# Performance work log

Hardware: AMD Instinct MI355X
Metric: run time of the kernel (lower is better)

Reference implementation:

```python
import jax, jax.numpy as jnp
import numpy as np

HID = 768          # args.hidden_size
LSTM2 = 768        # args.lstm_dim * 2
SCALE = HID ** -0.5


def _cross_attn(q_in, kv_in, Wq, bq, Wk, bk, Wv, bv):
    # Linear projections (weights stored as [in, out])
    Q = q_in @ Wq + bq            # [B, Sq, H]
    K = kv_in @ Wk + bk           # [B, Sk, H]
    V = kv_in @ Wv + bv           # [B, Sk, H]
    attn = jnp.einsum('bqh,bkh->bqk', Q, K) * SCALE
    attn = jax.nn.softmax(attn, axis=-1)
    return jnp.einsum('bqk,bkh->bqh', attn, V)


def setup_inputs() -> dict:
    key = jax.random.key(0)
    ks = jax.random.split(key, 14)
    B, Ssyn, Ssem = 4, 4096, 2048
    syntactic_feat = jax.random.normal(ks[0], (B, Ssyn, LSTM2), jnp.float32)
    semantic_feat = jax.random.normal(ks[1], (B, Ssem, HID), jnp.float32)

    def lin(k, fan_in, fan_out):
        kw, kb = jax.random.split(k)
        bound = 1.0 / np.sqrt(fan_in)
        W = jax.random.uniform(kw, (fan_in, fan_out), jnp.float32, -bound, bound)
        b = jax.random.uniform(kb, (fan_out,), jnp.float32, -bound, bound)
        return W, b

    # syntax_to_semantic: query_dim=HID, key_dim=LSTM2
    Wq1, bq1 = lin(ks[2], HID, HID)
    Wk1, bk1 = lin(ks[3], LSTM2, HID)
    Wv1, bv1 = lin(ks[4], LSTM2, HID)
    # semantic_to_syntax: query_dim=LSTM2, key_dim=HID
    Wq2, bq2 = lin(ks[5], LSTM2, HID)
    Wk2, bk2 = lin(ks[6], HID, HID)
    Wv2, bv2 = lin(ks[7], HID, HID)
    return dict(syntactic_feat=syntactic_feat, semantic_feat=semantic_feat,
                Wq1=Wq1, bq1=bq1, Wk1=Wk1, bk1=bk1, Wv1=Wv1, bv1=bv1,
                Wq2=Wq2, bq2=bq2, Wk2=Wk2, bk2=bk2, Wv2=Wv2, bv2=bv2)


def reference(syntactic_feat, semantic_feat,
              Wq1, bq1, Wk1, bk1, Wv1, bv1,
              Wq2, bq2, Wk2, bk2, Wv2, bv2):
    # enhanced_semantic: queries from semantic, keys/values from syntactic
    enhanced_semantic = _cross_attn(semantic_feat, syntactic_feat,
                                    Wq1, bq1, Wk1, bk1, Wv1, bv1)
    # enhanced_syntax: queries from syntactic, keys/values from semantic
    enhanced_syntax = _cross_attn(syntactic_feat, semantic_feat,
                                  Wq2, bq2, Wk2, bk2, Wv2, bv2)
    return enhanced_semantic, enhanced_syntax
```

## Files before the change

### kernel.cpp

```cpp
#include <hip/hip_runtime.h>
#include <stdint.h>


typedef unsigned short u16;
typedef __attribute__((ext_vector_type(8))) __bf16 bf16x8;
typedef __attribute__((ext_vector_type(4))) float f32x4;

__device__ __forceinline__ float bf2f(u16 u) {
  union { unsigned int i; float f; } x; x.i = ((unsigned int)u) << 16; return x.f;
}
__device__ __forceinline__ u16 f2bf(float f) {
  union { float f; unsigned int i; } x; x.f = f;
  unsigned int i = x.i;
  i += 0x7fffu + ((i >> 16) & 1u);
  return (u16)(i >> 16);
}

__device__ __forceinline__ void cp16(void* lds, const void* g) {
  __builtin_amdgcn_global_load_lds((__attribute__((address_space(1))) void*)g,
                                   (__attribute__((address_space(3))) void*)lds,
                                   16, 0, 0);
}

struct GemmDesc {
  const u16* A; const u16* Bt; const float* bias; void* C;
  long sA, sB, sC;
  int K, lda, ldb, ldc;
  int gx, gy;
  int start;
  int mode, outf;
  float scale;
};
struct GemmPack { GemmDesc d[6]; int nd; };

__global__ __launch_bounds__(256)
void gemm_multi_kernel(GemmPack p)
{
  __shared__ __align__(16) u16 Asl[128 * 64];
  __shared__ __align__(16) u16 Bsl[128 * 64];

  int seg = 0;
#pragma unroll
  for (int t = 1; t < 6; ++t)
    if (t < p.nd && (int)blockIdx.x >= p.d[t].start) seg = t;
  const GemmDesc& g = p.d[seg];
  const int local = (int)blockIdx.x - g.start;
  const int pxy = g.gx * g.gy;
  const int bz = local / pxy;
  const int rem = local - bz * pxy;
  const int by = rem / g.gx;
  const int bx = rem - by * g.gx;

  const int tid  = threadIdx.x;
  const int lane = tid & 63;
  const int wave = tid >> 6;
  const int l15  = lane & 15;
  const int quad = lane >> 4;
  const int mw   = (wave >> 1) * 64;
  const int nw   = (wave & 1) * 64;

  const char* Ab = (const char*)(g.A + (long)bz * g.sA + (long)bx * 128 * g.lda);
  const char* Bb = (const char*)(g.Bt + (long)bz * g.sB + (long)by * 128 * g.ldb);

  const int srow  = wave * 8 + (lane >> 3);
  const int gchk  = (lane & 7) ^ (lane >> 3);
  const long ldaB = (long)g.lda * 2;
  const long ldbB = (long)g.ldb * 2;
  const char* pa00 = Ab + (long)srow * ldaB + (gchk << 4);
  const char* pb00 = Bb + (long)srow * ldbB + (gchk << 4);
  char* ldsA = (char*)Asl + wave * 1024;
  char* ldsB = (char*)Bsl + wave * 1024;

  int ia[2][4], ib[2][4];
#pragma unroll
  for (int s = 0; s < 2; ++s)
#pragma unroll
    for (int i = 0; i < 4; ++i) {
      const int m = mw + i * 16 + l15;
      ia[s][i] = m * 8 + ((s * 4 + quad) ^ (l15 & 7));
      const int n = nw + i * 16 + l15;
      ib[s][i] = n * 8 + ((s * 4 + quad) ^ (l15 & 7));
    }

  f32x4 acc[4][4];
  {
    f32x4 zz = {0.f, 0.f, 0.f, 0.f};
#pragma unroll
    for (int i = 0; i < 4; ++i)
#pragma unroll
      for (int j = 0; j < 4; ++j) acc[i][j] = zz;
  }

  const int nk = g.K >> 6;
  for (int kk = 0; kk < nk; ++kk) {
    const long kb = (long)kk << 7;
#pragma unroll
    for (int r = 0; r < 4; ++r) {
      cp16(ldsA + r * 4096, pa00 + kb + (long)r * 32 * ldaB);
      cp16(ldsB + r * 4096, pb00 + kb + (long)r * 32 * ldbB);
    }
    __syncthreads();

    const bf16x8* As8 = (const bf16x8*)Asl;
    const bf16x8* Bs8 = (const bf16x8*)Bsl;
#pragma unroll
    for (int s = 0; s < 2; ++s) {
      bf16x8 a[4], b[4];
#pragma unroll
      for (int i = 0; i < 4; ++i) a[i] = As8[ia[s][i]];
#pragma unroll
      for (int j = 0; j < 4; ++j) b[j] = Bs8[ib[s][j]];
#pragma unroll
      for (int i = 0; i < 4; ++i)
#pragma unroll
        for (int j = 0; j < 4; ++j)
          acc[i][j] = __builtin_amdgcn_mfma_f32_16x16x32_bf16(b[j], a[i], acc[i][j], 0, 0, 0);
    }
    __syncthreads();
  }

  const long cbase = (long)bz * g.sC;
#pragma unroll
  for (int i = 0; i < 4; ++i) {
    const int row = bx * 128 + mw + i * 16 + l15;
    const float rbias = (g.mode == 2) ? g.bias[row] : 0.f;
#pragma unroll
    for (int j = 0; j < 4; ++j) {
      const int colbase = by * 128 + nw + j * 16 + quad * 4;
      float v[4];
#pragma unroll
      for (int r = 0; r < 4; ++r) v[r] = acc[i][j][r] * g.scale;
      if (g.mode == 1) {
        const float4 cb = *(const float4*)(g.bias + colbase);
        v[0] += cb.x; v[1] += cb.y; v[2] += cb.z; v[3] += cb.w;
      } else if (g.mode == 2) {
#pragma unroll
        for (int r = 0; r < 4; ++r) v[r] += rbias;
      }
      const long idx = cbase + (long)row * g.ldc + colbase;
      if (g.outf) {
        float4 st; st.x = v[0]; st.y = v[1]; st.z = v[2]; st.w = v[3];
        *(float4*)((float*)g.C + idx) = st;
      } else {
        uint2 st;
        st.x = (unsigned int)f2bf(v[0]) | ((unsigned int)f2bf(v[1]) << 16);
        st.y = (unsigned int)f2bf(v[2]) | ((unsigned int)f2bf(v[3]) << 16);
        *(uint2*)((u16*)g.C + idx) = st;
      }
    }
  }
}

__global__ __launch_bounds__(256)
void cvt2_bf16_kernel(const float* __restrict__ sa, u16* __restrict__ da, int n8a,
                      const float* __restrict__ sb, u16* __restrict__ db, int n8b)
{
  int idx = blockIdx.x * 256 + threadIdx.x;
  const float* src; u16* dst; int i;
  if (idx < n8a) { src = sa; dst = da; i = idx; }
  else           { src = sb; dst = db; i = idx - n8a; if (i >= n8b) return; }
  const float4* s4 = (const float4*)src;
  float4 a = s4[i * 2], b = s4[i * 2 + 1];
  uint4 o;
  o.x = (unsigned int)f2bf(a.x) | ((unsigned int)f2bf(a.y) << 16);
  o.y = (unsigned int)f2bf(a.z) | ((unsigned int)f2bf(a.w) << 16);
  o.z = (unsigned int)f2bf(b.x) | ((unsigned int)f2bf(b.y) << 16);
  o.w = (unsigned int)f2bf(b.z) | ((unsigned int)f2bf(b.w) << 16);
  ((uint4*)dst)[i] = o;
}

__global__ void transpose6_kernel(const float* s0, const float* s1, const float* s2,
                                  const float* s3, const float* s4, const float* s5,
                                  u16* d0, u16* d1, u16* d2,
                                  u16* d3, u16* d4, u16* d5)
{
  __shared__ float t[32][33];
  const float* src; u16* dst;
  switch (blockIdx.z) {
    case 0: src = s0; dst = d0; break;
    case 1: src = s1; dst = d1; break;
    case 2: src = s2; dst = d2; break;
    case 3: src = s3; dst = d3; break;
    case 4: src = s4; dst = d4; break;
    default: src = s5; dst = d5; break;
  }
  const int tx = threadIdx.x, ty = threadIdx.y;
  const int x = blockIdx.x * 32 + tx;
  const int y0 = blockIdx.y * 32;
#pragma unroll
  for (int j = 0; j < 32; j += 8) t[ty + j][tx] = src[(long)(y0 + ty + j) * 768 + x];
  __syncthreads();
  const int x2 = y0 + tx;
#pragma unroll
  for (int j = 0; j < 32; j += 8)
    dst[(long)(blockIdx.x * 32 + ty + j) * 768 + x2] = f2bf(t[tx][ty + j]);
}

template <int NV>
__device__ __forceinline__ void softmax_row(u16* row)
{
  __shared__ float red[8];
  const int tid  = threadIdx.x;
  const int lane = tid & 63;
  const int wave = tid >> 6;
  uint4* p4 = (uint4*)row;

  uint4 ld[NV / 8];
#pragma unroll
  for (int c = 0; c < NV / 8; ++c) ld[c] = p4[tid + c * 256];
  float v[NV];
#pragma unroll
  for (int c = 0; c < NV / 8; ++c) {
    unsigned int w[4] = {ld[c].x, ld[c].y, ld[c].z, ld[c].w};
#pragma unroll
    for (int q = 0; q < 4; ++q) {
      v[c * 8 + q * 2]     = bf2f((u16)(w[q] & 0xffffu));
      v[c * 8 + q * 2 + 1] = bf2f((u16)(w[q] >> 16));
    }
  }

  float m = -1e30f;
#pragma unroll
  for (int i = 0; i < NV; ++i) m = fmaxf(m, v[i]);
#pragma unroll
  for (int off = 32; off > 0; off >>= 1) m = fmaxf(m, __shfl_xor(m, off, 64));
  if (lane == 0) red[wave] = m;
  __syncthreads();
  m = fmaxf(fmaxf(red[0], red[1]), fmaxf(red[2], red[3]));

  float s = 0.f;
#pragma unroll
  for (int i = 0; i < NV; ++i) { v[i] = __expf(v[i] - m); s += v[i]; }
#pragma unroll
  for (int off = 32; off > 0; off >>= 1) s += __shfl_xor(s, off, 64);
  if (lane == 0) red[4 + wave] = s;
  __syncthreads();
  s = (red[4] + red[5]) + (red[6] + red[7]);
  const float inv = 1.0f / s;

#pragma unroll
  for (int c = 0; c < NV / 8; ++c) {
    unsigned int w[4];
#pragma unroll
    for (int q = 0; q < 4; ++q) {
      const u16 lo = f2bf(v[c * 8 + q * 2] * inv);
      const u16 hi = f2bf(v[c * 8 + q * 2 + 1] * inv);
      w[q] = (unsigned int)lo | ((unsigned int)hi << 16);
    }
    uint4 st; st.x = w[0]; st.y = w[1]; st.z = w[2]; st.w = w[3];
    p4[tid + c * 256] = st;
  }
}

__global__ __launch_bounds__(256)
void softmax_both_kernel(u16* S1, u16* S2, const u16* cpy_src, u16* cpy_dst)
{
  if (blockIdx.x < 8192) { softmax_row<16>(S1 + (long)blockIdx.x * 4096); return; }
  if (blockIdx.x < 24576) { softmax_row<8>(S2 + (long)(blockIdx.x - 8192) * 2048); return; }
  const long base = (long)(blockIdx.x - 24576) * 512 + threadIdx.x;
  const uint4* s = (const uint4*)cpy_src;
  uint4* d = (uint4*)cpy_dst;
  d[base] = s[base];
  d[base + 256] = s[base + 256];
}


static GemmDesc mkdesc(const void* A, const void* Bt, const float* bias, void* C,
                       long sA, long sB, long sC, int K, int lda, int ldb, int ldc,
                       int M, int N, int start, int mode, int outf, float scale)
{
  GemmDesc d;
  d.A = (const u16*)A; d.Bt = (const u16*)Bt; d.bias = bias; d.C = C;
  d.sA = sA; d.sB = sB; d.sC = sC;
  d.K = K; d.lda = lda; d.ldb = ldb; d.ldc = ldc;
  d.gx = M / 128; d.gy = N / 128; d.start = start;
  d.mode = mode; d.outf = outf; d.scale = scale;
  return d;
}

extern "C" void kernel_launch(void* const* d_in, const int* in_sizes, int n_in,
                              void* d_out, int out_size, void* d_ws, size_t ws_size,
                              hipStream_t stream)
{
  (void)in_sizes; (void)n_in; (void)out_size; (void)ws_size;
  const float* syn = (const float*)d_in[0];
  const float* sem = (const float*)d_in[1];
  const float* W[6]    = {(const float*)d_in[2], (const float*)d_in[4],  (const float*)d_in[6],
                          (const float*)d_in[8], (const float*)d_in[10], (const float*)d_in[12]};
  const float* bias[6] = {(const float*)d_in[3], (const float*)d_in[5],  (const float*)d_in[7],
                          (const float*)d_in[9], (const float*)d_in[11], (const float*)d_in[13]};
  float* out = (float*)d_out;

  u16* ws   = (u16*)d_ws;
  u16* S1   = ws;
  u16* synb = ws;
  u16* semb = ws + 12582912;
  u16* WT   = ws + 18874368;
  u16* S2   = ws + 33554432;
  u16* V1T  = ws + 67108864;
  u16* Q1   = ws + 79691776;
  u16* V2Tc = ws + 79691776;
  u16* K1  = (u16*)out;
  u16* o1  = (u16*)(out + 6291456);
  u16* Q2  = o1;
  u16* K2  = o1 + 12582912;
  u16* V2T = o1 + 18874368;

  const float SC = 0.036084391824351615f;

  cvt2_bf16_kernel<<<dim3(9216), dim3(256), 0, stream>>>(
      syn, synb, 1572864, sem, semb, 786432);

  transpose6_kernel<<<dim3(24, 24, 6), dim3(32, 8, 1), 0, stream>>>(
      W[0], W[1], W[2], W[3], W[4], W[5],
      WT + 0 * 589824, WT + 1 * 589824, WT + 2 * 589824,
      WT + 3 * 589824, WT + 4 * 589824, WT + 5 * 589824);

  {
    GemmPack p; p.nd = 6;
    p.d[0] = mkdesc(synb, WT + 1 * 589824, bias[1], K1, 0, 0, 0,
                    768, 768, 768, 768, 16384, 768, 0, 1, 0, 1.f);
    p.d[1] = mkdesc(synb, WT + 3 * 589824, bias[3], Q2, 0, 0, 0,
                    768, 768, 768, 768, 16384, 768, 768, 1, 0, 1.f);
    p.d[2] = mkdesc(WT + 2 * 589824, synb, bias[2], V1T, 0, 0, 0,
                    768, 768, 768, 16384, 768, 16384, 1536, 2, 0, 1.f);
    p.d[3] = mkdesc(semb, WT + 0 * 589824, bias[0], Q1, 0, 0, 0,
                    768, 768, 768, 768, 8192, 768, 2304, 1, 0, 1.f);
    p.d[4] = mkdesc(semb, WT + 4 * 589824, bias[4], K2, 0, 0, 0,
                    768, 768, 768, 768, 8192, 768, 2688, 1, 0, 1.f);
    p.d[5] = mkdesc(WT + 5 * 589824, semb, bias[5], V2T, 0, 0, 0,
                    768, 768, 768, 8192, 768, 8192, 3072, 2, 0, 1.f);
    gemm_multi_kernel<<<dim3(3456), dim3(256), 0, stream>>>(p);
  }

  {
    GemmPack p; p.nd = 2;
    p.d[0] = mkdesc(Q1, K1, nullptr, S1,
                    1572864L, 3145728L, 8388608L,
                    768, 768, 768, 4096, 2048, 4096, 0, 0, 0, SC);
    p.d[1] = mkdesc(Q2, K2, nullptr, S2,
                    3145728L, 1572864L, 8388608L,
                    768, 768, 768, 2048, 4096, 2048, 2048, 0, 0, SC);
    gemm_multi_kernel<<<dim3(4096), dim3(256), 0, stream>>>(p);
  }

  softmax_both_kernel<<<dim3(26112), dim3(256), 0, stream>>>(S1, S2, V2T, V2Tc);

  {
    GemmPack p; p.nd = 2;
    p.d[0] = mkdesc(S1, V1T, nullptr, out,
                    8388608L, 4096L, 1572864L,
                    4096, 4096, 16384, 768, 2048, 768, 0, 0, 1, 1.f);
    p.d[1] = mkdesc(S2, V2Tc, nullptr, out + 6291456,
                    8388608L, 2048L, 3145728L,
                    2048, 2048, 8192, 768, 4096, 768, 384, 0, 1, 1.f);
    gemm_multi_kernel<<<dim3(1152), dim3(256), 0, stream>>>(p);
  }
}
```

Baseline: 592.9 us.

## Replace 128x128 GEMM with 256x256 eight-wave double-buffered pipelined kernel

Swaps the 128x128-tile, 4-wave GEMM for a 256x256-tile, 8-wave kernel. It uses double-buffered LDS (128KB), async global-to-LDS loads interleaved with MFMA phases, explicit barriers and waitcnt, and setprio around the MFMA blocks. The larger tile cuts global traffic per FLOP, and the software pipeline overlaps loads with compute. The cost is fewer blocks per launch, which matters most for the final 288-block GEMM on a large-CU GPU, plus higher register and LDS pressure.

```diff
diff --git a/kernel.cpp b/kernel.cpp
--- a/kernel.cpp
+++ b/kernel.cpp
@@ -33,11 +33,41 @@
 };
 struct GemmPack { GemmDesc d[6]; int nd; };
 
-__global__ __launch_bounds__(256)
-void gemm_multi_kernel(GemmPack p)
-{
-  __shared__ __align__(16) u16 Asl[128 * 64];
-  __shared__ __align__(16) u16 Bsl[128 * 64];
+#define PHASE(MH, NH, PAR, STAGE, WAITC)                                      \
+  {                                                                           \
+    const bf16x8* As8 =                                                       \
+        (const bf16x8*)((const char*)L + (PAR) * 32768 + (MH) * 16384);       \
+    const bf16x8* Bs8 =                                                       \
+        (const bf16x8*)((const char*)L + 65536 + (PAR) * 32768 + (NH) * 16384);\
+    bf16x8 a0[2][4], b0[2][2];                                                \
+    _Pragma("unroll")                                                         \
+    for (int s = 0; s < 2; ++s) {                                             \
+      _Pragma("unroll")                                                       \
+      for (int i = 0; i < 4; ++i) a0[s][i] = As8[iaq[s][i]];                  \
+      _Pragma("unroll")                                                       \
+      for (int j = 0; j < 2; ++j) b0[s][j] = Bs8[ibq[s][j]];                  \
+    }                                                                         \
+    STAGE;                                                                    \
+    __builtin_amdgcn_s_barrier();                                             \
+    asm volatile("s_waitcnt lgkmcnt(0)" ::: "memory");                        \
+    __builtin_amdgcn_s_setprio(1);                                            \
+    _Pragma("unroll")                                                         \
+    for (int s = 0; s < 2; ++s)                                               \
+      _Pragma("unroll")                                                       \
+      for (int i = 0; i < 4; ++i)                                             \
+        _Pragma("unroll")                                                     \
+        for (int j = 0; j < 2; ++j)                                           \
+          acc[MH][NH][i][j] = __builtin_amdgcn_mfma_f32_16x16x32_bf16(        \
+              b0[s][j], a0[s][i], acc[MH][NH][i][j], 0, 0, 0);                \
+    __builtin_amdgcn_s_setprio(0);                                            \
+    WAITC;                                                                    \
+    __builtin_amdgcn_s_barrier();                                             \
+  }
+
+__global__ __launch_bounds__(512, 2)
+void gemm256_kernel(GemmPack p)
+{
+  __shared__ __align__(16) u16 L[65536];
 
   int seg = 0;
 #pragma unroll
@@ -56,96 +86,113 @@
   const int wave = tid >> 6;
   const int l15  = lane & 15;
   const int quad = lane >> 4;
-  const int mw   = (wave >> 1) * 64;
-  const int nw   = (wave & 1) * 64;
-
-  const char* Ab = (const char*)(g.A + (long)bz * g.sA + (long)bx * 128 * g.lda);
-  const char* Bb = (const char*)(g.Bt + (long)bz * g.sB + (long)by * 128 * g.ldb);
-
-  const int srow  = wave * 8 + (lane >> 3);
-  const int gchk  = (lane & 7) ^ (lane >> 3);
+  const int wm   = wave >> 2;
+  const int wn   = wave & 3;
+
+  const char* Ab = (const char*)(g.A + (long)bz * g.sA + (long)bx * 256 * g.lda);
+  const char* Bb = (const char*)(g.Bt + (long)bz * g.sB + (long)by * 256 * g.ldb);
   const long ldaB = (long)g.lda * 2;
   const long ldbB = (long)g.ldb * 2;
-  const char* pa00 = Ab + (long)srow * ldaB + (gchk << 4);
-  const char* pb00 = Bb + (long)srow * ldbB + (gchk << 4);
-  char* ldsA = (char*)Asl + wave * 1024;
-  char* ldsB = (char*)Bsl + wave * 1024;
-
-  int ia[2][4], ib[2][4];
-#pragma unroll
-  for (int s = 0; s < 2; ++s)
-#pragma unroll
-    for (int i = 0; i < 4; ++i) {
-      const int m = mw + i * 16 + l15;
-      ia[s][i] = m * 8 + ((s * 4 + quad) ^ (l15 & 7));
-      const int n = nw + i * 16 + l15;
-      ib[s][i] = n * 8 + ((s * 4 + quad) ^ (l15 & 7));
-    }
-
-  f32x4 acc[4][4];
+
+  const int gchk = (lane & 7) ^ (lane >> 3);
+  const char* pa0 = Ab + (long)(wave * 8 + (lane >> 3)) * ldaB + (gchk << 4);
+  const char* pb0 = Bb + (long)(wave * 8 + (lane >> 3)) * ldbB + (gchk << 4);
+  char* lA = (char*)L + wave * 1024;
+  char* lB = (char*)L + 65536 + wave * 1024;
+
+  auto stageA = [&](int par, int h, int kt) {
+    char* d = lA + par * 32768 + h * 16384;
+    const char* s = pa0 + (long)h * 128 * ldaB + ((long)kt << 7);
+    cp16(d, s);
+    cp16(d + 8192, s + 64 * ldaB);
+  };
+  auto stageB = [&](int par, int h, int kt) {
+    char* d = lB + par * 32768 + h * 16384;
+    const char* s = pb0 + (long)h * 128 * ldbB + ((long)kt << 7);
+    cp16(d, s);
+    cp16(d + 8192, s + 64 * ldbB);
+  };
+
+  int iaq[2][4], ibq[2][2];
+#pragma unroll
+  for (int s = 0; s < 2; ++s) {
+#pragma unroll
+    for (int i = 0; i < 4; ++i)
+      iaq[s][i] = (wm * 64 + i * 16 + l15) * 8 + ((s * 4 + quad) ^ (l15 & 7));
+#pragma unroll
+    for (int j = 0; j < 2; ++j)
+      ibq[s][j] = (wn * 32 + j * 16 + l15) * 8 + ((s * 4 + quad) ^ (l15 & 7));
+  }
+
+  f32x4 acc[2][2][4][2];
   {
     f32x4 zz = {0.f, 0.f, 0.f, 0.f};
 #pragma unroll
-    for (int i = 0; i < 4; ++i)
-#pragma unroll
-      for (int j = 0; j < 4; ++j) acc[i][j] = zz;
-  }
-
-  const int nk = g.K >> 6;
-  for (int kk = 0; kk < nk; ++kk) {
-    const long kb = (long)kk << 7;
-#pragma unroll
-    for (int r = 0; r < 4; ++r) {
-      cp16(ldsA + r * 4096, pa00 + kb + (long)r * 32 * ldaB);
-      cp16(ldsB + r * 4096, pb00 + kb + (long)r * 32 * ldbB);
-    }
-    __syncthreads();
-
-    const bf16x8* As8 = (const bf16x8*)Asl;
-    const bf16x8* Bs8 = (const bf16x8*)Bsl;
-#pragma unroll
-    for (int s = 0; s < 2; ++s) {
-      bf16x8 a[4], b[4];
-#pragma unroll
-      for (int i = 0; i < 4; ++i) a[i] = As8[ia[s][i]];
-#pragma unroll
-      for (int j = 0; j < 4; ++j) b[j] = Bs8[ib[s][j]];
-#pragma unroll
-      for (int i = 0; i < 4; ++i)
-#pragma unroll
-        for (int j = 0; j < 4; ++j)
-          acc[i][j] = __builtin_amdgcn_mfma_f32_16x16x32_bf16(b[j], a[i], acc[i][j], 0, 0, 0);
-    }
-    __syncthreads();
+    for (int mh = 0; mh < 2; ++mh)
+#pragma unroll
+      for (int nh = 0; nh < 2; ++nh)
+#pragma unroll
+        for (int i = 0; i < 4; ++i)
+#pragma unroll
+          for (int j = 0; j < 2; ++j) acc[mh][nh][i][j] = zz;
+  }
+
+  stageA(0, 0, 0); stageB(0, 0, 0);
+  stageA(0, 1, 0); stageB(0, 1, 0);
+  stageA(1, 0, 1); stageB(1, 0, 1);
+  asm volatile("s_waitcnt vmcnt(4)" ::: "memory");
+  __builtin_amdgcn_s_barrier();
+
+  const int NI = g.K >> 7;
+  for (int it = 0; it < NI; ++it) {
+    const int t = it * 2;
+    const bool more = (it + 1) < NI;
+    PHASE(0, 0, 0, stageA(1, 1, t + 1), )
+    PHASE(0, 1, 0, stageB(1, 1, t + 1), )
+    PHASE(1, 0, 0, if (more) stageA(0, 0, t + 2), )
+    PHASE(1, 1, 0, if (more) stageB(0, 0, t + 2),
+          if (more) { asm volatile("s_waitcnt vmcnt(4)" ::: "memory"); }
+          else      { asm volatile("s_waitcnt vmcnt(0)" ::: "memory"); })
+    PHASE(0, 0, 1, if (more) stageA(0, 1, t + 2), )
+    PHASE(0, 1, 1, if (more) stageB(0, 1, t + 2), )
+    PHASE(1, 0, 1, if (more) stageA(1, 0, t + 3), )
+    PHASE(1, 1, 1, if (more) stageB(1, 0, t + 3),
+          if (more) { asm volatile("s_waitcnt vmcnt(4)" ::: "memory"); })
   }
 
   const long cbase = (long)bz * g.sC;
 #pragma unroll
-  for (int i = 0; i < 4; ++i) {
-    const int row = bx * 128 + mw + i * 16 + l15;
-    const float rbias = (g.mode == 2) ? g.bias[row] : 0.f;
-#pragma unroll
-    for (int j = 0; j < 4; ++j) {
-      const int colbase = by * 128 + nw + j * 16 + quad * 4;
-      float v[4];
-#pragma unroll
-      for (int r = 0; r < 4; ++r) v[r] = acc[i][j][r] * g.scale;
-      if (g.mode == 1) {
-        const float4 cb = *(const float4*)(g.bias + colbase);
-        v[0] += cb.x; v[1] += cb.y; v[2] += cb.z; v[3] += cb.w;
-      } else if (g.mode == 2) {
-#pragma unroll
-        for (int r = 0; r < 4; ++r) v[r] += rbias;
-      }
-      const long idx = cbase + (long)row * g.ldc + colbase;
-      if (g.outf) {
-        float4 st; st.x = v[0]; st.y = v[1]; st.z = v[2]; st.w = v[3];
-        *(float4*)((float*)g.C + idx) = st;
-      } else {
-        uint2 st;
-        st.x = (unsigned int)f2bf(v[0]) | ((unsigned int)f2bf(v[1]) << 16);
-        st.y = (unsigned int)f2bf(v[2]) | ((unsigned int)f2bf(v[3]) << 16);
-        *(uint2*)((u16*)g.C + idx) = st;
+  for (int mh = 0; mh < 2; ++mh) {
+#pragma unroll
+    for (int i = 0; i < 4; ++i) {
+      const int row = bx * 256 + mh * 128 + wm * 64 + i * 16 + l15;
+      const float rbias = (g.mode == 2) ? g.bias[row] : 0.f;
+#pragma unroll
+      for (int nh = 0; nh < 2; ++nh) {
+#pragma unroll
+        for (int j = 0; j < 2; ++j) {
+          const int colbase = by * 256 + nh * 128 + wn * 32 + j * 16 + quad * 4;
+          float v[4];
+#pragma unroll
+          for (int r = 0; r < 4; ++r) v[r] = acc[mh][nh][i][j][r] * g.scale;
+          if (g.mode == 1) {
+            const float4 cb = *(const float4*)(g.bias + colbase);
+            v[0] += cb.x; v[1] += cb.y; v[2] += cb.z; v[3] += cb.w;
+          } else if (g.mode == 2) {
+#pragma unroll
+            for (int r = 0; r < 4; ++r) v[r] += rbias;
+          }
+          const long idx = cbase + (long)row * g.ldc + colbase;
+          if (g.outf) {
+            float4 st; st.x = v[0]; st.y = v[1]; st.z = v[2]; st.w = v[3];
+            *(float4*)((float*)g.C + idx) = st;
+          } else {
+            uint2 st;
+            st.x = (unsigned int)f2bf(v[0]) | ((unsigned int)f2bf(v[1]) << 16);
+            st.y = (unsigned int)f2bf(v[2]) | ((unsigned int)f2bf(v[3]) << 16);
+            *(uint2*)((u16*)g.C + idx) = st;
+          }
+        }
       }
     }
   }
@@ -273,7 +320,7 @@
   d.A = (const u16*)A; d.Bt = (const u16*)Bt; d.bias = bias; d.C = C;
   d.sA = sA; d.sB = sB; d.sC = sC;
   d.K = K; d.lda = lda; d.ldb = ldb; d.ldc = ldc;
-  d.gx = M / 128; d.gy = N / 128; d.start = start;
+  d.gx = M / 256; d.gy = N / 256; d.start = start;
   d.mode = mode; d.outf = outf; d.scale = scale;
   return d;
 }
@@ -321,16 +368,16 @@
     p.d[0] = mkdesc(synb, WT + 1 * 589824, bias[1], K1, 0, 0, 0,
                     768, 768, 768, 768, 16384, 768, 0, 1, 0, 1.f);
     p.d[1] = mkdesc(synb, WT + 3 * 589824, bias[3], Q2, 0, 0, 0,
-                    768, 768, 768, 768, 16384, 768, 768, 1, 0, 1.f);
+                    768, 768, 768, 768, 16384, 768, 192, 1, 0, 1.f);
     p.d[2] = mkdesc(WT + 2 * 589824, synb, bias[2], V1T, 0, 0, 0,
-                    768, 768, 768, 16384, 768, 16384, 1536, 2, 0, 1.f);
+                    768, 768, 768, 16384, 768, 16384, 384, 2, 0, 1.f);
     p.d[3] = mkdesc(semb, WT + 0 * 589824, bias[0], Q1, 0, 0, 0,
-                    768, 768, 768, 768, 8192, 768, 2304, 1, 0, 1.f);
+                    768, 768, 768, 768, 8192, 768, 576, 1, 0, 1.f);
     p.d[4] = mkdesc(semb, WT + 4 * 589824, bias[4], K2, 0, 0, 0,
-                    768, 768, 768, 768, 8192, 768, 2688, 1, 0, 1.f);
+                    768, 768, 768, 768, 8192, 768, 672, 1, 0, 1.f);
     p.d[5] = mkdesc(WT + 5 * 589824, semb, bias[5], V2T, 0, 0, 0,
-                    768, 768, 768, 8192, 768, 8192, 3072, 2, 0, 1.f);
-    gemm_multi_kernel<<<dim3(3456), dim3(256), 0, stream>>>(p);
+                    768, 768, 768, 8192, 768, 8192, 768, 2, 0, 1.f);
+    gemm256_kernel<<<dim3(864), dim3(512), 0, stream>>>(p);
   }
 
   {
@@ -340,8 +387,8 @@
                     768, 768, 768, 4096, 2048, 4096, 0, 0, 0, SC);
     p.d[1] = mkdesc(Q2, K2, nullptr, S2,
                     3145728L, 1572864L, 8388608L,
-                    768, 768, 768, 2048, 4096, 2048, 2048, 0, 0, SC);
-    gemm_multi_kernel<<<dim3(4096), dim3(256), 0, stream>>>(p);
+                    768, 768, 768, 2048, 4096, 2048, 512, 0, 0, SC);
+    gemm256_kernel<<<dim3(1024), dim3(512), 0, stream>>>(p);
   }
 
   softmax_both_kernel<<<dim3(26112), dim3(256), 0, stream>>>(S1, S2, V2T, V2Tc);
@@ -353,7 +400,7 @@
                     4096, 4096, 16384, 768, 2048, 768, 0, 0, 1, 1.f);
     p.d[1] = mkdesc(S2, V2Tc, nullptr, out + 6291456,
                     8388608L, 2048L, 3145728L,
-                    2048, 2048, 8192, 768, 4096, 768, 384, 0, 1, 1.f);
-    gemm_multi_kernel<<<dim3(1152), dim3(256), 0, stream>>>(p);
-  }
-}
+                    2048, 2048, 8192, 768, 4096, 768, 96, 0, 1, 1.f);
+    gemm256_kernel<<<dim3(288), dim3(512), 0, stream>>>(p);
+  }
+}
```

Result: no change. 600.9 us (+1.3%).
